# Performance work log

Hardware: AMD Instinct MI355X
Metric: run time of the kernel (lower is better)

## Reference

```python
import jax, jax.numpy as jnp
import numpy as np

N_ENT = 200000
N_REL = 500
D_MODEL = 512
BS = 256


def setup_inputs() -> dict:
    key = jax.random.key(0)
    k1, k2, k3, k4, k5, k6 = jax.random.split(key, 6)
    return {
        "s_ent": jax.random.randint(k1, (BS,), 0, N_ENT, dtype=jnp.int32),
        "relation": jax.random.randint(k2, (BS,), 0, N_REL, dtype=jnp.int32),
        "o_ent": jax.random.randint(k3, (BS,), 0, N_ENT, dtype=jnp.int32),
        "time": jax.random.randint(k4, (BS,), 0, 365, dtype=jnp.int32),
        "ent_emb": jax.random.normal(k5, (N_ENT, D_MODEL), dtype=jnp.float32),
        "rel_emb": jax.random.normal(k6, (N_REL, D_MODEL), dtype=jnp.float32),
    }


def reference(s_ent, relation, o_ent, time, ent_emb, rel_emb):
    # test_forward: scores = -||(e_s + r) - E_all||_2 for every entity.
    # Faithful math via the ||a-b||^2 = ||a||^2 - 2 a.b + ||b||^2 GEMM
    # decomposition, avoiding the [bs, n_ent, d] difference tensor.
    cond = ent_emb[s_ent] + rel_emb[relation]          # [bs, d]
    a2 = jnp.sum(cond * cond, axis=-1, keepdims=True)  # [bs, 1]
    b2 = jnp.sum(ent_emb * ent_emb, axis=-1)           # [n_ent]
    ab = jnp.einsum('bd,nd->bn', cond, ent_emb)        # [bs, n_ent]
    d2 = a2 - 2.0 * ab + b2[None, :]
    scores = -jnp.sqrt(jnp.maximum(d2, 1e-12))
    return scores
```

## Files before the change

kernel.cpp:

```cpp
#include <hip/hip_runtime.h>
#include <hip/hip_bf16.h>

typedef __attribute__((ext_vector_type(8))) short short8;
typedef __attribute__((ext_vector_type(4))) float f32x4;

#define D_MODEL 512
#define BN 64
#define NT 16
#define B_TILE 8192

__device__ __forceinline__ void gload16(const void* g, void* l) {
    typedef const __attribute__((address_space(1))) unsigned GT;
    typedef __attribute__((address_space(3))) unsigned LT;
    __builtin_amdgcn_global_load_lds((GT*)g, (LT*)l, 16, 0, 0);
}

__device__ __forceinline__ short f2bf(float f) {
    unsigned u = __builtin_bit_cast(unsigned, f);
    unsigned r = (u + 0x7fffu + ((u >> 16) & 1u)) >> 16;
    return (short)r;
}

__device__ __forceinline__ short8 cvt8(const f32x4& a, const f32x4& b) {
    union { __hip_bfloat162 h[4]; short8 s; } u;
    u.h[0] = __float22bfloat162_rn(make_float2(a[0], a[1]));
    u.h[1] = __float22bfloat162_rn(make_float2(a[2], a[3]));
    u.h[2] = __float22bfloat162_rn(make_float2(b[0], b[1]));
    u.h[3] = __float22bfloat162_rn(make_float2(b[2], b[3]));
    return u.s;
}

__global__ void prep_kernel(const int* __restrict__ s_ent, const int* __restrict__ rel,
                            const float* __restrict__ ent, const float* __restrict__ relemb,
                            short* __restrict__ condb, float* __restrict__ a2) {
    const int b = blockIdx.x;
    const int t = threadIdx.x;
    const float4 v = *(const float4*)(ent + (size_t)s_ent[b] * D_MODEL + t * 4);
    const float4 w = *(const float4*)(relemb + (size_t)rel[b] * D_MODEL + t * 4);
    float c0 = v.x + w.x, c1 = v.y + w.y, c2 = v.z + w.z, c3 = v.w + w.w;
    float sq = c0 * c0 + c1 * c1 + c2 * c2 + c3 * c3;

    short4 s;
    s.x = f2bf(c0); s.y = f2bf(c1); s.z = f2bf(c2); s.w = f2bf(c3);
    *(short4*)(condb + (size_t)b * D_MODEL + t * 4) = s;

    #pragma unroll
    for (int off = 1; off < 64; off <<= 1) sq += __shfl_xor(sq, off);
    __shared__ float red[2];
    if ((t & 63) == 0) red[t >> 6] = sq;
    __syncthreads();
    if (t == 0) a2[b] = red[0] + red[1];
}

__global__ __launch_bounds__(256, 4)
void score_kernel(const float* __restrict__ ent, const short* __restrict__ condb,
                  const float* __restrict__ a2, float* __restrict__ out, const int n_ent) {
    __shared__ __align__(16) unsigned char lds[3 * B_TILE];
    unsigned char* Bl = lds;

    const int tid  = threadIdx.x;
    const int lane = tid & 63;
    const int wm   = tid >> 6;
    const int lrow = lane & 15, g4 = lane >> 4;
    const long long nbase = (long long)blockIdx.x * BN;

    const int p0 = tid * 16, p1 = p0 + 4096;
    const int br0 = p0 >> 7, br1 = p1 >> 7;
    const long long gr0 = min(nbase + br0, (long long)(n_ent - 1));
    const long long gr1 = min(nbase + br1, (long long)(n_ent - 1));
    const char* gB0 = (const char*)ent + gr0 * 2048 + ((p0 & 127) ^ ((br0 & 7) << 4));
    const char* gB1 = (const char*)ent + gr1 * 2048 + ((p1 & 127) ^ ((br1 & 7) << 4));

    int boff0[4], boff1[4];
    #pragma unroll
    for (int f = 0; f < 4; ++f) {
        const int rb = f * 16 + lrow;
        const int sw = (rb & 7) << 4;
        boff0[f] = rb * 128 + ((g4 * 32) ^ sw);
        boff1[f] = rb * 128 + ((g4 * 32 + 16) ^ sw);
    }

    const short* abase = condb + (size_t)(wm * 64 + lrow) * D_MODEL + g4 * 8;

    f32x4 acc[4][4] = {};
    float sq[4] = {0.f, 0.f, 0.f, 0.f};

    gload16(gB0, Bl + p0);
    gload16(gB1, Bl + p1);
    gload16(gB0 + 128, Bl + B_TILE + p0);
    gload16(gB1 + 128, Bl + B_TILE + p1);

    #pragma unroll
    for (int t = 0; t < NT; ++t) {
        asm volatile("s_waitcnt vmcnt(2)" ::: "memory");
        __builtin_amdgcn_s_barrier();

        const short8 af0 = *(const short8*)(abase + t * 32);
        const short8 af1 = *(const short8*)(abase + t * 32 + 8192);
        const short8 af2 = *(const short8*)(abase + t * 32 + 16384);
        const short8 af3 = *(const short8*)(abase + t * 32 + 24576);

        if (t + 2 < NT) {
            unsigned char* bd = Bl + ((t + 2) % 3) * B_TILE;
            gload16(gB0 + (t + 2) * 128, bd + p0);
            gload16(gB1 + (t + 2) * 128, bd + p1);
        }

        const unsigned char* bb = Bl + (t % 3) * B_TILE;
        #pragma unroll
        for (int fn = 0; fn < 4; ++fn) {
            const f32x4 v0 = *(const f32x4*)(bb + boff0[fn]);
            const f32x4 v1 = *(const f32x4*)(bb + boff1[fn]);
            if (wm == 0)
                sq[fn] += v0[0]*v0[0] + v0[1]*v0[1] + v0[2]*v0[2] + v0[3]*v0[3]
                        + v1[0]*v1[0] + v1[1]*v1[1] + v1[2]*v1[2] + v1[3]*v1[3];
            const short8 bf = cvt8(v0, v1);
            acc[0][fn] = __builtin_amdgcn_mfma_f32_16x16x32_bf16(af0, bf, acc[0][fn], 0, 0, 0);
            acc[1][fn] = __builtin_amdgcn_mfma_f32_16x16x32_bf16(af1, bf, acc[1][fn], 0, 0, 0);
            acc[2][fn] = __builtin_amdgcn_mfma_f32_16x16x32_bf16(af2, bf, acc[2][fn], 0, 0, 0);
            acc[3][fn] = __builtin_amdgcn_mfma_f32_16x16x32_bf16(af3, bf, acc[3][fn], 0, 0, 0);
        }
    }

    float* b2s = (float*)(lds + B_TILE);
    if (wm == 0) {
        #pragma unroll
        for (int fn = 0; fn < 4; ++fn) {
            sq[fn] += __shfl_xor(sq[fn], 16);
            sq[fn] += __shfl_xor(sq[fn], 32);
        }
        if (lane < 16) {
            #pragma unroll
            for (int fn = 0; fn < 4; ++fn) b2s[fn * 16 + lane] = sq[fn];
        }
    }
    __syncthreads();

    #pragma unroll
    for (int fm = 0; fm < 4; ++fm) {
        const int m0 = wm * 64 + fm * 16 + g4 * 4;
        const f32x4 a2v = *(const f32x4*)(a2 + m0);
        #pragma unroll
        for (int fn = 0; fn < 4; ++fn) {
            const int nl = fn * 16 + lrow;
            const long long ng = nbase + nl;
            if (ng < n_ent) {
                const float b2v = b2s[nl];
                #pragma unroll
                for (int r = 0; r < 4; ++r) {
                    float d2 = a2v[r] - 2.f * acc[fm][fn][r] + b2v;
                    out[(size_t)(m0 + r) * n_ent + ng] = -sqrtf(fmaxf(d2, 1e-12f));
                }
            }
        }
    }
}

extern "C" void kernel_launch(void* const* d_in, const int* in_sizes, int n_in,
                              void* d_out, int out_size, void* d_ws, size_t ws_size,
                              hipStream_t stream) {
    const int*   s_ent  = (const int*)d_in[0];
    const int*   rel    = (const int*)d_in[1];
    const float* ent    = (const float*)d_in[4];
    const float* relemb = (const float*)d_in[5];
    float* out = (float*)d_out;

    const int bs    = in_sizes[0];
    const int n_ent = in_sizes[4] / D_MODEL;

    short* condb = (short*)d_ws;
    float* a2    = (float*)((char*)d_ws + (size_t)bs * D_MODEL * 2);

    prep_kernel<<<bs, 128, 0, stream>>>(s_ent, rel, ent, relemb, condb, a2);

    const int ntiles = (n_ent + BN - 1) / BN;
    score_kernel<<<ntiles, 256, 0, stream>>>(ent, condb, a2, out, n_ent);
}
```

Measured before the change: 197.6 us.

## Widen entity tile to 128 with 8 waves and 4-stage 256B-chunk pipeline

Each score block now covers 128 entities with 512 threads (8 waves split 4x2 over batch and entity), instead of 64 entities with 256 threads. Each LDS stage holds a 64-float chunk of the reduction dimension across a 4-buffer ring with three stages in flight, and the loop is fully unrolled into 8 steps with explicit vmcnt waits. The aim is fewer, larger blocks, deeper prefetch, and fewer barriers per K step. In exchange LDS use rises to about 128KB per block, which limits occupancy to one block per CU.

```diff
diff --git a/kernel.cpp b/kernel.cpp
--- a/kernel.cpp
+++ b/kernel.cpp
@@ -5,9 +5,8 @@
 typedef __attribute__((ext_vector_type(4))) float f32x4;
 
 #define D_MODEL 512
-#define BN 64
-#define NT 16
-#define B_TILE 8192
+#define BN 128
+#define S_TILE 32768
 
 __device__ __forceinline__ void gload16(const void* g, void* l) {
     typedef const __attribute__((address_space(1))) unsigned GT;
@@ -52,32 +51,38 @@
     if (t == 0) a2[b] = red[0] + red[1];
 }
 
-__global__ __launch_bounds__(256, 4)
+__global__ __launch_bounds__(512, 2)
 void score_kernel(const float* __restrict__ ent, const short* __restrict__ condb,
                   const float* __restrict__ a2, float* __restrict__ out, const int n_ent) {
-    __shared__ __align__(16) unsigned char lds[3 * B_TILE];
-    unsigned char* Bl = lds;
+    __shared__ __align__(16) unsigned char Qb[4][S_TILE];
+    __shared__ float b2s[BN];
 
     const int tid  = threadIdx.x;
     const int lane = tid & 63;
-    const int wm   = tid >> 6;
+    const int w    = tid >> 6, wm = w >> 1, wn = w & 1;
     const int lrow = lane & 15, g4 = lane >> 4;
     const long long nbase = (long long)blockIdx.x * BN;
 
-    const int p0 = tid * 16, p1 = p0 + 4096;
-    const int br0 = p0 >> 7, br1 = p1 >> 7;
-    const long long gr0 = min(nbase + br0, (long long)(n_ent - 1));
-    const long long gr1 = min(nbase + br1, (long long)(n_ent - 1));
-    const char* gB0 = (const char*)ent + gr0 * 2048 + ((p0 & 127) ^ ((br0 & 7) << 4));
-    const char* gB1 = (const char*)ent + gr1 * 2048 + ((p1 & 127) ^ ((br1 & 7) << 4));
+    const int r0   = tid >> 4;
+    const int col0 = (tid * 16) & 255;
+    const int swz0 = (r0 & 7) << 4;
+    const char* gsrc[4];
+    int ldso[4];
+    #pragma unroll
+    for (int j = 0; j < 4; ++j) {
+        const int row = r0 + j * 32;
+        const long long grow = min(nbase + row, (long long)(n_ent - 1));
+        gsrc[j] = (const char*)ent + grow * 2048 + (col0 ^ swz0);
+        ldso[j] = tid * 16 + j * 8192;
+    }
 
-    int boff0[4], boff1[4];
+    int off0[4], off1[4];
     #pragma unroll
     for (int f = 0; f < 4; ++f) {
-        const int rb = f * 16 + lrow;
+        const int rb = wn * 64 + f * 16 + lrow;
         const int sw = (rb & 7) << 4;
-        boff0[f] = rb * 128 + ((g4 * 32) ^ sw);
-        boff1[f] = rb * 128 + ((g4 * 32 + 16) ^ sw);
+        off0[f] = rb * 256 + ((g4 * 32) ^ sw);
+        off1[f] = rb * 256 + ((g4 * 32 + 16) ^ sw);
     }
 
     const short* abase = condb + (size_t)(wm * 64 + lrow) * D_MODEL + g4 * 8;
@@ -85,44 +90,55 @@
     f32x4 acc[4][4] = {};
     float sq[4] = {0.f, 0.f, 0.f, 0.f};
 
-    gload16(gB0, Bl + p0);
-    gload16(gB1, Bl + p1);
-    gload16(gB0 + 128, Bl + B_TILE + p0);
-    gload16(gB1 + 128, Bl + B_TILE + p1);
+    #pragma unroll
+    for (int j = 0; j < 4; ++j) gload16(gsrc[j],       Qb[0] + ldso[j]);
+    #pragma unroll
+    for (int j = 0; j < 4; ++j) gload16(gsrc[j] + 256, Qb[1] + ldso[j]);
+    #pragma unroll
+    for (int j = 0; j < 4; ++j) gload16(gsrc[j] + 512, Qb[2] + ldso[j]);
 
-    #pragma unroll
-    for (int t = 0; t < NT; ++t) {
-        asm volatile("s_waitcnt vmcnt(2)" ::: "memory");
-        __builtin_amdgcn_s_barrier();
+#define STEP(T, VM, DO_ISSUE)                                                              \
+  {                                                                                        \
+    asm volatile("s_waitcnt vmcnt(" #VM ")" ::: "memory");                                 \
+    __builtin_amdgcn_s_barrier();                                                          \
+    if (DO_ISSUE) {                                                                        \
+      unsigned char* bd = Qb[((T) + 3) & 3];                                               \
+      _Pragma("unroll")                                                                    \
+      for (int j = 0; j < 4; ++j) gload16(gsrc[j] + ((T) + 3) * 256, bd + ldso[j]);        \
+    }                                                                                      \
+    const unsigned char* bb = Qb[(T) & 3];                                                 \
+    _Pragma("unroll")                                                                      \
+    for (int s = 0; s < 2; ++s) {                                                          \
+      const short8 af0 = *(const short8*)(abase + ((T) * 2 + s) * 32);                     \
+      const short8 af1 = *(const short8*)(abase + ((T) * 2 + s) * 32 + 8192);              \
+      const short8 af2 = *(const short8*)(abase + ((T) * 2 + s) * 32 + 16384);             \
+      const short8 af3 = *(const short8*)(abase + ((T) * 2 + s) * 32 + 24576);             \
+      _Pragma("unroll")                                                                    \
+      for (int fn = 0; fn < 4; ++fn) {                                                     \
+        const f32x4 v0 = *(const f32x4*)(bb + off0[fn] + s * 128);                         \
+        const f32x4 v1 = *(const f32x4*)(bb + off1[fn] + s * 128);                         \
+        if (wm == 0)                                                                       \
+          sq[fn] += v0[0]*v0[0] + v0[1]*v0[1] + v0[2]*v0[2] + v0[3]*v0[3]                  \
+                  + v1[0]*v1[0] + v1[1]*v1[1] + v1[2]*v1[2] + v1[3]*v1[3];                 \
+        const short8 bf = cvt8(v0, v1);                                                    \
+        acc[0][fn] = __builtin_amdgcn_mfma_f32_16x16x32_bf16(af0, bf, acc[0][fn], 0, 0, 0);\
+        acc[1][fn] = __builtin_amdgcn_mfma_f32_16x16x32_bf16(af1, bf, acc[1][fn], 0, 0, 0);\
+        acc[2][fn] = __builtin_amdgcn_mfma_f32_16x16x32_bf16(af2, bf, acc[2][fn], 0, 0, 0);\
+        acc[3][fn] = __builtin_amdgcn_mfma_f32_16x16x32_bf16(af3, bf, acc[3][fn], 0, 0, 0);\
+      }                                                                                    \
+    }                                                                                      \
+  }
 
-        const short8 af0 = *(const short8*)(abase + t * 32);
-        const short8 af1 = *(const short8*)(abase + t * 32 + 8192);
-        const short8 af2 = *(const short8*)(abase + t * 32 + 16384);
-        const short8 af3 = *(const short8*)(abase + t * 32 + 24576);
+    STEP(0, 8, true)
+    STEP(1, 8, true)
+    STEP(2, 8, true)
+    STEP(3, 8, true)
+    STEP(4, 8, true)
+    STEP(5, 8, false)
+    STEP(6, 4, false)
+    STEP(7, 0, false)
+#undef STEP
 
-        if (t + 2 < NT) {
-            unsigned char* bd = Bl + ((t + 2) % 3) * B_TILE;
-            gload16(gB0 + (t + 2) * 128, bd + p0);
-            gload16(gB1 + (t + 2) * 128, bd + p1);
-        }
-
-        const unsigned char* bb = Bl + (t % 3) * B_TILE;
-        #pragma unroll
-        for (int fn = 0; fn < 4; ++fn) {
-            const f32x4 v0 = *(const f32x4*)(bb + boff0[fn]);
-            const f32x4 v1 = *(const f32x4*)(bb + boff1[fn]);
-            if (wm == 0)
-                sq[fn] += v0[0]*v0[0] + v0[1]*v0[1] + v0[2]*v0[2] + v0[3]*v0[3]
-                        + v1[0]*v1[0] + v1[1]*v1[1] + v1[2]*v1[2] + v1[3]*v1[3];
-            const short8 bf = cvt8(v0, v1);
-            acc[0][fn] = __builtin_amdgcn_mfma_f32_16x16x32_bf16(af0, bf, acc[0][fn], 0, 0, 0);
-            acc[1][fn] = __builtin_amdgcn_mfma_f32_16x16x32_bf16(af1, bf, acc[1][fn], 0, 0, 0);
-            acc[2][fn] = __builtin_amdgcn_mfma_f32_16x16x32_bf16(af2, bf, acc[2][fn], 0, 0, 0);
-            acc[3][fn] = __builtin_amdgcn_mfma_f32_16x16x32_bf16(af3, bf, acc[3][fn], 0, 0, 0);
-        }
-    }
-
-    float* b2s = (float*)(lds + B_TILE);
     if (wm == 0) {
         #pragma unroll
         for (int fn = 0; fn < 4; ++fn) {
@@ -131,7 +147,7 @@
         }
         if (lane < 16) {
             #pragma unroll
-            for (int fn = 0; fn < 4; ++fn) b2s[fn * 16 + lane] = sq[fn];
+            for (int fn = 0; fn < 4; ++fn) b2s[wn * 64 + fn * 16 + lane] = sq[fn];
         }
     }
     __syncthreads();
@@ -142,7 +158,7 @@
         const f32x4 a2v = *(const f32x4*)(a2 + m0);
         #pragma unroll
         for (int fn = 0; fn < 4; ++fn) {
-            const int nl = fn * 16 + lrow;
+            const int nl = wn * 64 + fn * 16 + lrow;
             const long long ng = nbase + nl;
             if (ng < n_ent) {
                 const float b2v = b2s[nl];
@@ -174,5 +190,5 @@
     prep_kernel<<<bs, 128, 0, stream>>>(s_ent, rel, ent, relemb, condb, a2);
 
     const int ntiles = (n_ent + BN - 1) / BN;
-    score_kernel<<<ntiles, 256, 0, stream>>>(ent, condb, a2, out, n_ent);
+    score_kernel<<<ntiles, 512, 0, stream>>>(ent, condb, a2, out, n_ent);
 }
```

Result: slower. 248.0 us (+25.5%).
